# Optimization experiments

Measured on AMD Instinct MI355X. Metric: run time of the kernel, lower is better.

Reference implementation:

```python
import jax, jax.numpy as jnp
import numpy as np

DIM = 180
WS = 16        # window_size
OWS = 24       # overlap_win_size = int(16*0.5)+16
HEADS = 6
HD = DIM // HEADS
MLP_HID = DIM * 2
TABLE = (WS + OWS - 1) ** 2  # 1521
H = W = 256
B = 1


def layernorm(x, g, b, eps=1e-5):
    mu = x.mean(-1, keepdims=True)
    d = x - mu
    var = (d * d).mean(-1, keepdims=True)
    return g * d / jnp.sqrt(var + eps) + b


def setup_inputs() -> dict:
    key = jax.random.key(0)
    ks = jax.random.split(key, 12)
    std = 0.02
    inp = {
        'x': jax.random.normal(ks[0], (B, H * W, DIM), jnp.float32),
        'rpi': jax.random.randint(ks[1], (WS * WS, OWS * OWS), 0, TABLE, jnp.int32),
        'h': H,
        'w': W,
        'norm1_g': jnp.ones((DIM,), jnp.float32),
        'norm1_b': jnp.zeros((DIM,), jnp.float32),
        'q_w': jax.random.normal(ks[2], (DIM, DIM), jnp.float32) * std,
        'q_b': jnp.zeros((DIM,), jnp.float32),
        'kv_w': jax.random.normal(ks[3], (DIM, 2 * DIM), jnp.float32) * std,
        'kv_b': jnp.zeros((2 * DIM,), jnp.float32),
        'rpb_table': jax.random.normal(ks[4], (TABLE, HEADS), jnp.float32) * std,
        'proj_w': jax.random.normal(ks[5], (DIM, DIM), jnp.float32) * std,
        'proj_b': jnp.zeros((DIM,), jnp.float32),
        'norm2_g': jnp.ones((DIM,), jnp.float32),
        'norm2_b': jnp.zeros((DIM,), jnp.float32),
        'mlp_w1': jax.random.normal(ks[6], (DIM, MLP_HID), jnp.float32) * std,
        'mlp_b1': jnp.zeros((MLP_HID,), jnp.float32),
        'mlp_w2': jax.random.normal(ks[7], (MLP_HID, DIM), jnp.float32) * std,
        'mlp_b2': jnp.zeros((DIM,), jnp.float32),
    }
    return inp


def reference(x, rpi, h, w, norm1_g, norm1_b, q_w, q_b, kv_w, kv_b,
              rpb_table, proj_w, proj_b, norm2_g, norm2_b,
              mlp_w1, mlp_b1, mlp_w2, mlp_b2):
    b, L, c = x.shape
    ws, ows, heads = WS, OWS, HEADS
    d = c // heads
    scale = d ** -0.5
    pad = (ows - ws) // 2  # 4
    nh, nw = h // ws, w // ws
    nq, n = ws * ws, ows * ows
    b_ = b * nh * nw

    shortcut = x
    xn = layernorm(x, norm1_g, norm1_b)
    x_img = xn.reshape(b, h, w, c)

    q = x_img @ q_w + q_b                    # [b,h,w,c]
    kv = x_img @ kv_w + kv_b                 # [b,h,w,2c] (k | v)

    # window_partition for q -> [b_, nq, c]
    qw = q.reshape(b, nh, ws, nw, ws, c).transpose(0, 1, 3, 2, 4, 5)
    qw = qw.reshape(b_, nq, c)

    # nn.Unfold(kernel=ows, stride=ws, padding=pad) on kv -> overlapping windows
    kvp = jnp.pad(kv, ((0, 0), (pad, pad), (pad, pad), (0, 0)))
    rows = (jnp.arange(nh) * ws)[:, None] + jnp.arange(ows)   # [nh, ows]
    cols = (jnp.arange(nw) * ws)[:, None] + jnp.arange(ows)   # [nw, ows]
    t = kvp[:, rows]                         # [b, nh, ows, W+2p, 2c]
    t = t[:, :, :, cols]                     # [b, nh, ows, nw, ows, 2c]
    t = t.transpose(0, 1, 3, 2, 4, 5).reshape(b_, n, 2 * c)
    k_win, v_win = t[..., :c], t[..., c:]

    qh = qw.reshape(b_, nq, heads, d).transpose(0, 2, 1, 3) * scale
    kh = k_win.reshape(b_, n, heads, d).transpose(0, 2, 1, 3)
    vh = v_win.reshape(b_, n, heads, d).transpose(0, 2, 1, 3)

    attn = jnp.einsum('bhqd,bhkd->bhqk', qh, kh)              # [b_,heads,nq,n]
    bias = rpb_table[rpi.reshape(-1)].reshape(nq, n, heads).transpose(2, 0, 1)
    attn = jax.nn.softmax(attn + bias[None], axis=-1)
    out = jnp.einsum('bhqk,bhkd->bhqd', attn, vh)
    out = out.transpose(0, 2, 1, 3).reshape(b_, nq, c)

    # window_reverse -> [b, h*w, c]
    xo = out.reshape(b, nh, nw, ws, ws, c).transpose(0, 1, 3, 2, 4, 5)
    xo = xo.reshape(b, h * w, c)

    xo = xo @ proj_w + proj_b + shortcut
    xn2 = layernorm(xo, norm2_g, norm2_b)
    mlp = jax.nn.gelu(xn2 @ mlp_w1 + mlp_b1, approximate=False) @ mlp_w2 + mlp_b2
    return xo + mlp
```

## Files before the change

kernel.cpp:

```cpp
#include <hip/hip_runtime.h>
#include <hip/hip_bf16.h>
#include <stdint.h>

#define DIM 180
#define WS 16
#define OWS 24
#define HEADS 6
#define HD 30
#define MLP_HID 360
#define HH 256
#define WW 256
#define L (HH * WW)
#define NWIN 256
#define NQ 256
#define NK 576

#define KP1 192
#define KP2 384
#define NQKV 576

#define QSCALE 0.2633988734672831f
#define LOG2E 1.4426950408889634f

typedef float f4v __attribute__((ext_vector_type(4)));
typedef short s8v __attribute__((ext_vector_type(8)));
typedef short s4v __attribute__((ext_vector_type(4)));

static __device__ __forceinline__ short f2bf(float x) {
    union { __hip_bfloat16 h; short s; } u;
    u.h = __float2bfloat16(x);
    return u.s;
}
static __device__ __forceinline__ uint32_t pack_bf2(float lo, float hi) {
    union { __hip_bfloat162 h; uint32_t u; } u;
    u.h.x = __float2bfloat16(lo);
    u.h.y = __float2bfloat16(hi);
    return u.u;
}

typedef __attribute__((address_space(1))) const unsigned int ga_u32;
typedef __attribute__((address_space(3))) unsigned int la_u32;
static __device__ __forceinline__ void gld16(const void* g, void* l) {
    __builtin_amdgcn_global_load_lds((ga_u32*)g, (la_u32*)l, 16, 0, 0);
}

__global__ __launch_bounds__(64) void ln_kernel(const float* __restrict__ x,
                                                const float* __restrict__ g,
                                                const float* __restrict__ b,
                                                __hip_bfloat16* __restrict__ out) {
    int row = blockIdx.x;
    int t = threadIdx.x;
    const float* xr = x + (size_t)row * DIM;
    float v0 = xr[t];
    float v1 = xr[t + 64];
    float v2 = (t < DIM - 128) ? xr[t + 128] : 0.f;
    float s = v0 + v1 + v2;
    #pragma unroll
    for (int o = 32; o > 0; o >>= 1) s += __shfl_down(s, o);
    s = __shfl(s, 0);
    float mu = s * (1.f / DIM);
    float d0 = v0 - mu, d1 = v1 - mu;
    float d2 = (t < DIM - 128) ? (v2 - mu) : 0.f;
    float vs = d0 * d0 + d1 * d1 + d2 * d2;
    #pragma unroll
    for (int o = 32; o > 0; o >>= 1) vs += __shfl_down(vs, o);
    vs = __shfl(vs, 0);
    float rstd = rsqrtf(vs * (1.f / DIM) + 1e-5f);
    __hip_bfloat16* orow = out + (size_t)row * KP1;
    orow[t]      = __float2bfloat16(g[t] * d0 * rstd + b[t]);
    orow[t + 64] = __float2bfloat16(g[t + 64] * d1 * rstd + b[t + 64]);
    if (t < DIM - 128)
        orow[t + 128] = __float2bfloat16(g[t + 128] * d2 * rstd + b[t + 128]);
    if (t < KP1 - DIM) orow[DIM + t] = __float2bfloat16(0.f);
}

__global__ __launch_bounds__(256) void bias_kernel(const int* __restrict__ rpi,
                                                   const float* __restrict__ rpb,
                                                   float* __restrict__ biasC) {
    int idx = blockIdx.x * 256 + threadIdx.x;
    int j = idx & 15;
    int q = (idx >> 4) & 255;
    int r = idx >> 12;
    int kc = r % 36;
    int head = r / 36;
    int k = (kc >> 1) * 32 + ((j >> 2) << 3) + ((kc & 1) << 2) + (j & 3);
    int t = rpi[q * NK + k];
    biasC[idx] = rpb[t * HEADS + head] * LOG2E;
}

__global__ __launch_bounds__(256) void wconv_kernel(
        const float* __restrict__ qw, const float* __restrict__ kvw,
        const float* __restrict__ pw, const float* __restrict__ w1,
        const float* __restrict__ w2, short* __restrict__ wt) {
    int idx = blockIdx.x * 256 + threadIdx.x;
    float v = 0.f;
    if (idx < 110592) {
        int n = idx / KP1, k = idx - n * KP1;
        if (k < DIM) {
            if (n < DIM) v = qw[k * DIM + n] * QSCALE;
            else if (n < 540) v = kvw[k * (2 * DIM) + (n - DIM)];
        }
    } else if (idx < 147456) {
        int r = idx - 110592;
        int n = r / KP1, k = r - n * KP1;
        if (k < DIM && n < DIM) v = pw[k * DIM + n];
    } else if (idx < 221184) {
        int r = idx - 147456;
        int n = r / KP1, k = r - n * KP1;
        if (k < DIM && n < MLP_HID) v = w1[k * MLP_HID + n];
    } else {
        int r = idx - 221184;
        int n = r / KP2, k = r - n * KP2;
        if (k < MLP_HID && n < DIM) v = w2[k * DIM + n];
    }
    wt[idx] = f2bf(v);
}

__global__ __launch_bounds__(256) void bconv_kernel(
        const float* __restrict__ qb, const float* __restrict__ kvb,
        const float* __restrict__ pb, const float* __restrict__ b1,
        const float* __restrict__ b2, float* __restrict__ bv) {
    int idx = blockIdx.x * 256 + threadIdx.x;
    if (idx >= 1344) return;
    float v = 0.f;
    if (idx < 576) {
        if (idx < DIM) v = qb[idx] * QSCALE;
        else if (idx < 540) v = kvb[idx - DIM];
    } else if (idx < 768) {
        int n = idx - 576; if (n < DIM) v = pb[n];
    } else if (idx < 1152) {
        int n = idx - 768; if (n < MLP_HID) v = b1[n];
    } else {
        int n = idx - 1152; if (n < DIM) v = b2[n];
    }
    bv[idx] = v;
}

__global__ __launch_bounds__(256) void mgemm(
        const short* __restrict__ A, const short* __restrict__ Wt,
        const float* __restrict__ bias,
        float* __restrict__ outf, short* __restrict__ outb,
        int lda, int ldo, int nK, int mode) {
    __shared__ short As[2][128 * 32];
    __shared__ short Wsm[2][64 * 32];
    int tid = threadIdx.x;
    int lane = tid & 63, wave = tid >> 6;
    int q15 = lane & 15, quad = lane >> 4;
    int n0 = blockIdx.x * 64;
    int m0 = blockIdx.y * 128;

    auto stage = [&](int buf, int k0) {
        int lr = lane >> 2, c = lane & 3;
        const short* Ab = A + (size_t)m0 * lda + k0;
        #pragma unroll
        for (int i = 0; i < 2; i++) {
            int r = i * 64 + wave * 16 + lr;
            gld16(Ab + (size_t)r * lda + ((c ^ (r & 3)) * 8),
                  &As[buf][(i * 64 + wave * 16) * 32]);
        }
        const short* Wb = Wt + (size_t)n0 * lda + k0;
        {
            int r = wave * 16 + lr;
            gld16(Wb + (size_t)r * lda + ((c ^ (r & 3)) * 8),
                  &Wsm[buf][(wave * 16) * 32]);
        }
    };

    f4v acc[2][4];
    #pragma unroll
    for (int a = 0; a < 2; a++)
        #pragma unroll
        for (int b = 0; b < 4; b++) acc[a][b] = (f4v){0.f, 0.f, 0.f, 0.f};

    stage(0, 0);
    __syncthreads();
    for (int ch = 0; ch < nK; ch++) {
        int buf = ch & 1;
        if (ch + 1 < nK) stage(buf ^ 1, (ch + 1) * 32);
        s8v af[2], wf[4];
        #pragma unroll
        for (int mt = 0; mt < 2; mt++) {
            int r = wave * 32 + mt * 16 + q15;
            af[mt] = *(const s8v*)&As[buf][r * 32 + ((quad ^ (r & 3)) * 8)];
        }
        #pragma unroll
        for (int nt = 0; nt < 4; nt++) {
            int r = nt * 16 + q15;
            wf[nt] = *(const s8v*)&Wsm[buf][r * 32 + ((quad ^ (r & 3)) * 8)];
        }
        #pragma unroll
        for (int mt = 0; mt < 2; mt++)
            #pragma unroll
            for (int nt = 0; nt < 4; nt++)
                acc[mt][nt] = __builtin_amdgcn_mfma_f32_16x16x32_bf16(
                    af[mt], wf[nt], acc[mt][nt], 0, 0, 0);
        __syncthreads();
    }

    #pragma unroll
    for (int mt = 0; mt < 2; mt++) {
        int mb = m0 + wave * 32 + mt * 16 + quad * 4;
        #pragma unroll
        for (int nt = 0; nt < 4; nt++) {
            int n = n0 + nt * 16 + q15;
            float bv = bias[n];
            f4v a = acc[mt][nt];
            #pragma unroll
            for (int r = 0; r < 4; r++) {
                int m = mb + r;
                float v = a[r] + bv;
                if (mode == 0) {
                    outb[(size_t)m * ldo + n] = f2bf(v);
                } else if (mode == 1) {
                    float ge = 0.5f * v * (1.f + erff(v * 0.70710678118654752f));
                    outb[(size_t)m * ldo + n] = f2bf(ge);
                } else {
                    if (n < DIM) outf[(size_t)m * DIM + n] += v;
                }
            }
        }
    }
}

__global__ __launch_bounds__(256) void projln(
        const short* __restrict__ A, const short* __restrict__ Wt,
        const float* __restrict__ bias, const float* __restrict__ resid,
        const float* __restrict__ g2, const float* __restrict__ b2,
        float* __restrict__ outf, short* __restrict__ outb) {
    __shared__ short As[2][64 * 32];
    __shared__ short Wsm[2][192 * 32];
    int tid = threadIdx.x;
    int lane = tid & 63, wave = tid >> 6;
    int q15 = lane & 15, quad = lane >> 4;
    int m0 = blockIdx.x * 64;

    auto stage = [&](int buf, int k0) {
        int lr = lane >> 2, c = lane & 3;
        const short* Ab = A + (size_t)m0 * KP1 + k0;
        {
            int r = wave * 16 + lr;
            gld16(Ab + (size_t)r * KP1 + ((c ^ (r & 3)) * 8),
                  &As[buf][(wave * 16) * 32]);
        }
        #pragma unroll
        for (int i = 0; i < 3; i++) {
            int r = i * 64 + wave * 16 + lr;
            gld16(Wt + (size_t)r * KP1 + k0 + ((c ^ (r & 3)) * 8),
                  &Wsm[buf][(i * 64 + wave * 16) * 32]);
        }
    };

    f4v acc[12];
    #pragma unroll
    for (int b = 0; b < 12; b++) acc[b] = (f4v){0.f, 0.f, 0.f, 0.f};

    stage(0, 0);
    __syncthreads();
    for (int ch = 0; ch < KP1 / 32; ch++) {
        int buf = ch & 1;
        if (ch + 1 < KP1 / 32) stage(buf ^ 1, (ch + 1) * 32);
        int ra = wave * 16 + q15;
        s8v af = *(const s8v*)&As[buf][ra * 32 + ((quad ^ (ra & 3)) * 8)];
        #pragma unroll
        for (int nt = 0; nt < 12; nt++) {
            int r = nt * 16 + q15;
            s8v wf = *(const s8v*)&Wsm[buf][r * 32 + ((quad ^ (r & 3)) * 8)];
            acc[nt] = __builtin_amdgcn_mfma_f32_16x16x32_bf16(af, wf, acc[nt], 0, 0, 0);
        }
        __syncthreads();
    }

    float gv[12], bv[12], biasv[12];
    #pragma unroll
    for (int nt = 0; nt < 12; nt++) {
        int n = nt * 16 + q15;
        biasv[nt] = bias[n];
        gv[nt] = (n < DIM) ? g2[n] : 0.f;
        bv[nt] = (n < DIM) ? b2[n] : 0.f;
    }
    int mb = m0 + wave * 16 + quad * 4;
    #pragma unroll
    for (int r = 0; r < 4; r++) {
        int m = mb + r;
        float v[12];
        float s = 0.f, ss = 0.f;
        #pragma unroll
        for (int nt = 0; nt < 12; nt++) {
            int n = nt * 16 + q15;
            float x = acc[nt][r] + biasv[nt];
            if (n < DIM) x += resid[(size_t)m * DIM + n];
            else x = 0.f;
            v[nt] = x;
            s += x;
            ss += x * x;
        }
        #pragma unroll
        for (int o = 8; o > 0; o >>= 1) {
            s += __shfl_xor(s, o);
            ss += __shfl_xor(ss, o);
        }
        float mu = s * (1.f / DIM);
        float var = ss * (1.f / DIM) - mu * mu;
        float rstd = rsqrtf(var + 1e-5f);
        #pragma unroll
        for (int nt = 0; nt < 12; nt++) {
            int n = nt * 16 + q15;
            if (n < DIM) outf[(size_t)m * DIM + n] = v[nt];
            outb[(size_t)m * KP1 + n] = f2bf(gv[nt] * (v[nt] - mu) * rstd + bv[nt]);
        }
    }
}

#define CHUNK 32
#define NCHUNK (NK / CHUNK)

__global__ __launch_bounds__(256) void attn_kernel(
        const __hip_bfloat16* __restrict__ qkvb,
        const float* __restrict__ biasC, __hip_bfloat16* __restrict__ aout) {
    __shared__ __align__(16) short Ks[2][CHUNK][32];
    __shared__ __align__(16) short Vt[2][32][40];

    int tid = threadIdx.x;
    int lane = tid & 63;
    int wave = tid >> 6;
    int q15 = lane & 15;
    int quad = lane >> 4;
    int bid = blockIdx.x;
    int grp = bid / 48;
    int r48 = bid - grp * 48;
    int head = r48 >> 3;
    int win = grp * 8 + (r48 & 7);
    int bh = win >> 4, bw = win & 15;

    const uint32_t* kvd = (const uint32_t*)qkvb;

    s8v qf[4];
    #pragma unroll
    for (int qt = 0; qt < 4; qt++) {
        int q = wave * 64 + qt * 16 + q15;
        int qy = q >> 4, qx = q & 15;
        size_t pos = (size_t)(bh * WS + qy) * WW + (bw * WS + qx);
        const uint32_t* qp = kvd + pos * 288 + head * 15 + quad * 4;
        uint32_t w0 = qp[0], w1 = qp[1], w2 = qp[2], w3 = qp[3];
        union { uint32_t u[4]; s8v v; } cv;
        cv.u[0] = w0; cv.u[1] = w1; cv.u[2] = w2; cv.u[3] = w3;
        qf[qt] = cv.v;
    }
    if (head == 0) {
        int qy = tid >> 4, qx = tid & 15;
        size_t pos = (size_t)(bh * WS + qy) * WW + (bw * WS + qx);
        uint2 z = make_uint2(0u, 0u);
        uint2* oz = (uint2*)(aout + pos * KP1 + DIM);
        oz[0] = z; oz[1] = z; oz[2] = z;
    }

    int keyK = tid >> 3, pK = tid & 7;
    int keyV = tid & 31, pp = tid >> 5;

    auto rowbase = [&](int jk) -> const uint32_t* {
        int oy = jk / OWS, ox = jk - oy * OWS;
        int y = bh * WS - 4 + oy, x = bw * WS - 4 + ox;
        if ((unsigned)y < HH && (unsigned)x < WW)
            return kvd + ((size_t)y * WW + x) * 288;
        return nullptr;
    };
    auto loadKV = [&](int c0, uint32_t& ka, uint32_t& kb, uint32_t& va, uint32_t& vb) {
        ka = kb = va = vb = 0u;
        const uint32_t* rk = rowbase(c0 + keyK);
        if (rk) {
            const uint32_t* kp = rk + 90 + head * 15 + pK * 2;
            ka = kp[0];
            if (pK < 7) kb = kp[1];
        }
        const uint32_t* rv = rowbase(c0 + keyV);
        if (rv) {
            const uint32_t* vp = rv + 180 + head * 15 + pp * 2;
            va = vp[0];
            if (pp < 7) vb = vp[1];
        }
    };
    auto writeKV = [&](int bufi, uint32_t ka, uint32_t kb, uint32_t va, uint32_t vb) {
        *(uint2*)&Ks[bufi][keyK][pK * 4] = make_uint2(ka, kb);
        int d0 = pp * 4;
        Vt[bufi][d0][keyV]     = (short)(va & 0xffff);
        Vt[bufi][d0 + 1][keyV] = (short)(va >> 16);
        if (pp < 7) {
            Vt[bufi][d0 + 2][keyV] = (short)(vb & 0xffff);
            Vt[bufi][d0 + 3][keyV] = (short)(vb >> 16);
        } else {
            Vt[bufi][30][keyV] = (short)0x3F80;
            Vt[bufi][31][keyV] = 0;
        }
    };

    const float* bC  = biasC + (size_t)head * (36 * 256 * 16);
    const float* bCl = bC + ((size_t)(wave * 64 + q15)) * 16 + quad * 4;
    f4v cb[2][4];
    auto loadBias = [&](int ch) {
        #pragma unroll
        for (int kt = 0; kt < 2; kt++)
            #pragma unroll
            for (int qt = 0; qt < 4; qt++)
                cb[kt][qt] = *(const f4v*)(bCl + ((size_t)(ch * 2 + kt) * 256 + qt * 16) * 16);
    };

    uint32_t kaA, kbA, vaA, vbA;
    uint32_t kaB, kbB, vaB, vbB;

    loadKV(0,     kaA, kbA, vaA, vbA);
    loadKV(CHUNK, kaB, kbB, vaB, vbB);
    loadBias(0);
    writeKV(0, kaA, kbA, vaA, vbA);
    __syncthreads();

    f4v oacc[2][4];
    #pragma unroll
    for (int a = 0; a < 2; a++)
        #pragma unroll
        for (int b = 0; b < 4; b++) oacc[a][b] = (f4v){0.f, 0.f, 0.f, 0.f};

    int pr = ((q15 & 12) << 1) | (q15 & 3);

    auto body = [&](int ch, int bufR,
                    uint32_t& kaR, uint32_t& kbR, uint32_t& vaR, uint32_t& vbR,
                    uint32_t& kaW, uint32_t& kbW, uint32_t& vaW, uint32_t& vbW) {
        s8v kf0 = *(const s8v*)&Ks[bufR][pr][quad * 8];
        s8v kf1 = *(const s8v*)&Ks[bufR][pr + 4][quad * 8];
        s8v va0 = *(const s8v*)&Vt[bufR][q15][quad * 8];
        s8v va1 = *(const s8v*)&Vt[bufR][16 + q15][quad * 8];

        #pragma unroll
        for (int qt = 0; qt < 4; qt++) {
            cb[0][qt] = __builtin_amdgcn_mfma_f32_16x16x32_bf16(kf0, qf[qt], cb[0][qt], 0, 0, 0);
            cb[1][qt] = __builtin_amdgcn_mfma_f32_16x16x32_bf16(kf1, qf[qt], cb[1][qt], 0, 0, 0);
        }
        if (ch + 2 < NCHUNK) loadKV((ch + 2) * CHUNK, kaR, kbR, vaR, vbR);

        s8v pbv[4];
        #pragma unroll
        for (int qt = 0; qt < 4; qt++) {
            union { uint32_t u[4]; s8v v; } pk;
            pk.u[0] = pack_bf2(__builtin_amdgcn_exp2f(cb[0][qt][0]), __builtin_amdgcn_exp2f(cb[0][qt][1]));
            pk.u[1] = pack_bf2(__builtin_amdgcn_exp2f(cb[0][qt][2]), __builtin_amdgcn_exp2f(cb[0][qt][3]));
            pk.u[2] = pack_bf2(__builtin_amdgcn_exp2f(cb[1][qt][0]), __builtin_amdgcn_exp2f(cb[1][qt][1]));
            pk.u[3] = pack_bf2(__builtin_amdgcn_exp2f(cb[1][qt][2]), __builtin_amdgcn_exp2f(cb[1][qt][3]));
            pbv[qt] = pk.v;
        }
        if (ch + 1 < NCHUNK) loadBias(ch + 1);

        #pragma unroll
        for (int qt = 0; qt < 4; qt++) {
            oacc[0][qt] = __builtin_amdgcn_mfma_f32_16x16x32_bf16(va0, pbv[qt], oacc[0][qt], 0, 0, 0);
            oacc[1][qt] = __builtin_amdgcn_mfma_f32_16x16x32_bf16(va1, pbv[qt], oacc[1][qt], 0, 0, 0);
        }

        if (ch + 1 < NCHUNK) writeKV(bufR ^ 1, kaW, kbW, vaW, vbW);

        asm volatile("s_waitcnt lgkmcnt(0)" ::: "memory");
        __builtin_amdgcn_sched_barrier(0);
        __builtin_amdgcn_s_barrier();
    };

    #pragma unroll 1
    for (int t = 0; t < NCHUNK / 2; t++) {
        body(2 * t,     0, kaA, kbA, vaA, vbA, kaB, kbB, vaB, vbB);
        body(2 * t + 1, 1, kaB, kbB, vaB, vbB, kaA, kbA, vaA, vbA);
    }

    #pragma unroll
    for (int nt = 0; nt < 4; nt++) {
        float l = __shfl(oacc[1][nt][2], 48 | q15);
        float rl = 1.0f / l;
        int q = wave * 64 + nt * 16 + q15;
        int qy = q >> 4, qx = q & 15;
        size_t pos = (size_t)(bh * WS + qy) * WW + (bw * WS + qx);
        uint32_t* od = (uint32_t*)(aout + pos * KP1 + head * HD);
        int dh = quad * 2;
        f4v o0 = oacc[0][nt], o1 = oacc[1][nt];
        od[dh]     = pack_bf2(o0[0] * rl, o0[1] * rl);
        od[dh + 1] = pack_bf2(o0[2] * rl, o0[3] * rl);
        od[8 + dh] = pack_bf2(o1[0] * rl, o1[1] * rl);
        if (quad < 3)
            od[8 + dh + 1] = pack_bf2(o1[2] * rl, o1[3] * rl);
    }
}

extern "C" void kernel_launch(void* const* d_in, const int* in_sizes, int n_in,
                              void* d_out, int out_size, void* d_ws, size_t ws_size,
                              hipStream_t stream) {
    const float* x      = (const float*)d_in[0];
    const int*   rpi    = (const int*)d_in[1];
    const float* n1g    = (const float*)d_in[4];
    const float* n1b    = (const float*)d_in[5];
    const float* q_w    = (const float*)d_in[6];
    const float* q_b    = (const float*)d_in[7];
    const float* kv_w   = (const float*)d_in[8];
    const float* kv_b   = (const float*)d_in[9];
    const float* rpb    = (const float*)d_in[10];
    const float* proj_w = (const float*)d_in[11];
    const float* proj_b = (const float*)d_in[12];
    const float* n2g    = (const float*)d_in[13];
    const float* n2b    = (const float*)d_in[14];
    const float* w1     = (const float*)d_in[15];
    const float* b1     = (const float*)d_in[16];
    const float* w2     = (const float*)d_in[17];
    const float* b2     = (const float*)d_in[18];
    float* out = (float*)d_out;

    char* ws = (char*)d_ws;
    short* qkvb  = (short*)(ws);
    short* xn    = (short*)(ws + 75497472ull);
    float* biasC = (float*)(ws + 100663296ull);
    short* wt    = (short*)(ws + 104202240ull);
    short* wt_qkv  = wt;
    short* wt_proj = wt + 110592;
    short* wt_1    = wt + 147456;
    short* wt_2    = wt + 221184;
    float* bvec  = (float*)(ws + 104202240ull + 589824ull);
    float* b_qkv  = bvec;
    float* b_proj = bvec + 576;
    float* b_1    = bvec + 768;
    float* b_2    = bvec + 1152;
    short* ao  = xn;
    short* xn2 = qkvb;
    short* h1  = qkvb + 12582912;

    bias_kernel<<<884736 / 256, 256, 0, stream>>>(rpi, rpb, biasC);
    wconv_kernel<<<294912 / 256, 256, 0, stream>>>(q_w, kv_w, proj_w, w1, w2, wt);
    bconv_kernel<<<6, 256, 0, stream>>>(q_b, kv_b, proj_b, b1, b2, bvec);
    ln_kernel<<<L, 64, 0, stream>>>(x, n1g, n1b, (__hip_bfloat16*)xn);
    mgemm<<<dim3(NQKV / 64, L / 128), 256, 0, stream>>>(
        xn, wt_qkv, b_qkv, nullptr, qkvb, KP1, NQKV, KP1 / 32, 0);
    attn_kernel<<<NWIN * HEADS, 256, 0, stream>>>(
        (const __hip_bfloat16*)qkvb, biasC, (__hip_bfloat16*)ao);
    projln<<<L / 64, 256, 0, stream>>>(
        ao, wt_proj, b_proj, x, n2g, n2b, out, xn2);
    mgemm<<<dim3(KP2 / 64, L / 128), 256, 0, stream>>>(
        xn2, wt_1, b_1, nullptr, h1, KP1, KP2, KP1 / 32, 1);
    mgemm<<<dim3(KP1 / 64, L / 128), 256, 0, stream>>>(
        h1, wt_2, b_2, out, nullptr, KP2, 0, KP2 / 32, 3);
}
```

Before: 411.7 us.

## Widen attention to 512 threads, bf16 bias, tanh GELU, batched layernorm

The attention kernel now runs 8 waves of 32 queries each and processes 64-key chunks. The K shared-memory layout gets an XOR swizzle and the bias is added after the QK MFMA instead of being used as the accumulator. The precomputed bias table is stored as bf16, halving its traffic. GELU switches from exact erf to the tanh approximation computed with exp2, and layernorm packs four rows per 256-thread block. The tanh GELU and bf16 bias add numerical error relative to the exact reference.

```diff
diff --git a/kernel.cpp b/kernel.cpp
--- a/kernel.cpp
+++ b/kernel.cpp
@@ -37,6 +37,12 @@
     u.h.y = __float2bfloat16(hi);
     return u.u;
 }
+static __device__ __forceinline__ float bflo(uint32_t u) {
+    union { uint32_t i; float f; } c; c.i = u << 16; return c.f;
+}
+static __device__ __forceinline__ float bfhi(uint32_t u) {
+    union { uint32_t i; float f; } c; c.i = u & 0xffff0000u; return c.f;
+}
 
 typedef __attribute__((address_space(1))) const unsigned int ga_u32;
 typedef __attribute__((address_space(3))) unsigned int la_u32;
@@ -44,12 +50,12 @@
     __builtin_amdgcn_global_load_lds((ga_u32*)g, (la_u32*)l, 16, 0, 0);
 }
 
-__global__ __launch_bounds__(64) void ln_kernel(const float* __restrict__ x,
-                                                const float* __restrict__ g,
-                                                const float* __restrict__ b,
-                                                __hip_bfloat16* __restrict__ out) {
-    int row = blockIdx.x;
-    int t = threadIdx.x;
+__global__ __launch_bounds__(256) void ln_kernel(const float* __restrict__ x,
+                                                 const float* __restrict__ g,
+                                                 const float* __restrict__ b,
+                                                 __hip_bfloat16* __restrict__ out) {
+    int row = blockIdx.x * 4 + (threadIdx.x >> 6);
+    int t = threadIdx.x & 63;
     const float* xr = x + (size_t)row * DIM;
     float v0 = xr[t];
     float v1 = xr[t + 64];
@@ -76,7 +82,7 @@
 
 __global__ __launch_bounds__(256) void bias_kernel(const int* __restrict__ rpi,
                                                    const float* __restrict__ rpb,
-                                                   float* __restrict__ biasC) {
+                                                   ushort* __restrict__ biasC) {
     int idx = blockIdx.x * 256 + threadIdx.x;
     int j = idx & 15;
     int q = (idx >> 4) & 255;
@@ -85,7 +91,7 @@
     int head = r / 36;
     int k = (kc >> 1) * 32 + ((j >> 2) << 3) + ((kc & 1) << 2) + (j & 3);
     int t = rpi[q * NK + k];
-    biasC[idx] = rpb[t * HEADS + head] * LOG2E;
+    biasC[idx] = (ushort)f2bf(rpb[t * HEADS + head] * LOG2E);
 }
 
 __global__ __launch_bounds__(256) void wconv_kernel(
@@ -212,8 +218,10 @@
                 if (mode == 0) {
                     outb[(size_t)m * ldo + n] = f2bf(v);
                 } else if (mode == 1) {
-                    float ge = 0.5f * v * (1.f + erff(v * 0.70710678118654752f));
-                    outb[(size_t)m * ldo + n] = f2bf(ge);
+                    float y = 0.7978845608028654f * (v + 0.044715f * v * v * v);
+                    float e = __builtin_amdgcn_exp2f(y * 2.885390081777927f);
+                    float th = 1.f - 2.f / (1.f + e);
+                    outb[(size_t)m * ldo + n] = f2bf(0.5f * v * (1.f + th));
                 } else {
                     if (n < DIM) outf[(size_t)m * DIM + n] += v;
                 }
@@ -311,14 +319,14 @@
     }
 }
 
-#define CHUNK 32
+#define CHUNK 64
 #define NCHUNK (NK / CHUNK)
 
-__global__ __launch_bounds__(256) void attn_kernel(
+__global__ __launch_bounds__(512) void attn_kernel(
         const __hip_bfloat16* __restrict__ qkvb,
-        const float* __restrict__ biasC, __hip_bfloat16* __restrict__ aout) {
+        const ushort* __restrict__ biasC, __hip_bfloat16* __restrict__ aout) {
     __shared__ __align__(16) short Ks[2][CHUNK][32];
-    __shared__ __align__(16) short Vt[2][32][40];
+    __shared__ __align__(16) short Vt[2][2][32][40];
 
     int tid = threadIdx.x;
     int lane = tid & 63;
@@ -334,10 +342,10 @@
 
     const uint32_t* kvd = (const uint32_t*)qkvb;
 
-    s8v qf[4];
-    #pragma unroll
-    for (int qt = 0; qt < 4; qt++) {
-        int q = wave * 64 + qt * 16 + q15;
+    s8v qf[2];
+    #pragma unroll
+    for (int qt = 0; qt < 2; qt++) {
+        int q = wave * 32 + qt * 16 + q15;
         int qy = q >> 4, qx = q & 15;
         size_t pos = (size_t)(bh * WS + qy) * WW + (bw * WS + qx);
         const uint32_t* qp = kvd + pos * 288 + head * 15 + quad * 4;
@@ -346,7 +354,7 @@
         cv.u[0] = w0; cv.u[1] = w1; cv.u[2] = w2; cv.u[3] = w3;
         qf[qt] = cv.v;
     }
-    if (head == 0) {
+    if (head == 0 && tid < 256) {
         int qy = tid >> 4, qx = tid & 15;
         size_t pos = (size_t)(bh * WS + qy) * WW + (bw * WS + qx);
         uint2 z = make_uint2(0u, 0u);
@@ -355,7 +363,9 @@
     }
 
     int keyK = tid >> 3, pK = tid & 7;
-    int keyV = tid & 31, pp = tid >> 5;
+    int keyV = tid & 63, pp = tid >> 6;
+    int gV = keyV >> 5, kv32 = keyV & 31;
+    int pKs = pK ^ (((keyK >> 3) & 3) << 1);
 
     auto rowbase = [&](int jk) -> const uint32_t* {
         int oy = jk / OWS, ox = jk - oy * OWS;
@@ -380,28 +390,28 @@
         }
     };
     auto writeKV = [&](int bufi, uint32_t ka, uint32_t kb, uint32_t va, uint32_t vb) {
-        *(uint2*)&Ks[bufi][keyK][pK * 4] = make_uint2(ka, kb);
+        *(uint2*)&Ks[bufi][keyK][pKs * 4] = make_uint2(ka, kb);
         int d0 = pp * 4;
-        Vt[bufi][d0][keyV]     = (short)(va & 0xffff);
-        Vt[bufi][d0 + 1][keyV] = (short)(va >> 16);
+        Vt[bufi][gV][d0][kv32]     = (short)(va & 0xffff);
+        Vt[bufi][gV][d0 + 1][kv32] = (short)(va >> 16);
         if (pp < 7) {
-            Vt[bufi][d0 + 2][keyV] = (short)(vb & 0xffff);
-            Vt[bufi][d0 + 3][keyV] = (short)(vb >> 16);
+            Vt[bufi][gV][d0 + 2][kv32] = (short)(vb & 0xffff);
+            Vt[bufi][gV][d0 + 3][kv32] = (short)(vb >> 16);
         } else {
-            Vt[bufi][30][keyV] = (short)0x3F80;
-            Vt[bufi][31][keyV] = 0;
-        }
-    };
-
-    const float* bC  = biasC + (size_t)head * (36 * 256 * 16);
-    const float* bCl = bC + ((size_t)(wave * 64 + q15)) * 16 + quad * 4;
-    f4v cb[2][4];
+            Vt[bufi][gV][30][kv32] = (short)0x3F80;
+            Vt[bufi][gV][31][kv32] = 0;
+        }
+    };
+
+    const char* bBase = (const char*)biasC +
+        ((size_t)head * (36 * 256 * 16) + (size_t)(wave * 32 + q15) * 16 + quad * 4) * 2;
+    uint2 bb[4][2];
     auto loadBias = [&](int ch) {
         #pragma unroll
-        for (int kt = 0; kt < 2; kt++)
+        for (int kt = 0; kt < 4; kt++)
             #pragma unroll
-            for (int qt = 0; qt < 4; qt++)
-                cb[kt][qt] = *(const f4v*)(bCl + ((size_t)(ch * 2 + kt) * 256 + qt * 16) * 16);
+            for (int qt = 0; qt < 2; qt++)
+                bb[kt][qt] = *(const uint2*)(bBase + (size_t)(ch * 4 + kt) * 8192 + qt * 512);
     };
 
     uint32_t kaA, kbA, vaA, vbA;
@@ -413,46 +423,66 @@
     writeKV(0, kaA, kbA, vaA, vbA);
     __syncthreads();
 
-    f4v oacc[2][4];
+    f4v oacc[2][2];
     #pragma unroll
     for (int a = 0; a < 2; a++)
         #pragma unroll
-        for (int b = 0; b < 4; b++) oacc[a][b] = (f4v){0.f, 0.f, 0.f, 0.f};
+        for (int b = 0; b < 2; b++) oacc[a][b] = (f4v){0.f, 0.f, 0.f, 0.f};
 
     int pr = ((q15 & 12) << 1) | (q15 & 3);
+    int rslot = (quad ^ (q15 >> 2)) * 8;
 
     auto body = [&](int ch, int bufR,
                     uint32_t& kaR, uint32_t& kbR, uint32_t& vaR, uint32_t& vbR,
                     uint32_t& kaW, uint32_t& kbW, uint32_t& vaW, uint32_t& vbW) {
-        s8v kf0 = *(const s8v*)&Ks[bufR][pr][quad * 8];
-        s8v kf1 = *(const s8v*)&Ks[bufR][pr + 4][quad * 8];
-        s8v va0 = *(const s8v*)&Vt[bufR][q15][quad * 8];
-        s8v va1 = *(const s8v*)&Vt[bufR][16 + q15][quad * 8];
-
-        #pragma unroll
-        for (int qt = 0; qt < 4; qt++) {
-            cb[0][qt] = __builtin_amdgcn_mfma_f32_16x16x32_bf16(kf0, qf[qt], cb[0][qt], 0, 0, 0);
-            cb[1][qt] = __builtin_amdgcn_mfma_f32_16x16x32_bf16(kf1, qf[qt], cb[1][qt], 0, 0, 0);
-        }
+        s8v kf[4];
+        #pragma unroll
+        for (int kt = 0; kt < 4; kt++)
+            kf[kt] = *(const s8v*)&Ks[bufR][(kt >> 1) * 32 + pr + (kt & 1) * 4][rslot];
+        s8v va[2][2];
+        #pragma unroll
+        for (int g = 0; g < 2; g++) {
+            va[0][g] = *(const s8v*)&Vt[bufR][g][q15][quad * 8];
+            va[1][g] = *(const s8v*)&Vt[bufR][g][16 + q15][quad * 8];
+        }
+
+        f4v zf = (f4v){0.f, 0.f, 0.f, 0.f};
+        f4v s[2][4];
+        #pragma unroll
+        for (int qt = 0; qt < 2; qt++)
+            #pragma unroll
+            for (int kt = 0; kt < 4; kt++)
+                s[qt][kt] = __builtin_amdgcn_mfma_f32_16x16x32_bf16(kf[kt], qf[qt], zf, 0, 0, 0);
+
         if (ch + 2 < NCHUNK) loadKV((ch + 2) * CHUNK, kaR, kbR, vaR, vbR);
 
-        s8v pbv[4];
-        #pragma unroll
-        for (int qt = 0; qt < 4; qt++) {
-            union { uint32_t u[4]; s8v v; } pk;
-            pk.u[0] = pack_bf2(__builtin_amdgcn_exp2f(cb[0][qt][0]), __builtin_amdgcn_exp2f(cb[0][qt][1]));
-            pk.u[1] = pack_bf2(__builtin_amdgcn_exp2f(cb[0][qt][2]), __builtin_amdgcn_exp2f(cb[0][qt][3]));
-            pk.u[2] = pack_bf2(__builtin_amdgcn_exp2f(cb[1][qt][0]), __builtin_amdgcn_exp2f(cb[1][qt][1]));
-            pk.u[3] = pack_bf2(__builtin_amdgcn_exp2f(cb[1][qt][2]), __builtin_amdgcn_exp2f(cb[1][qt][3]));
-            pbv[qt] = pk.v;
-        }
+        s8v pbv[2][2];
+        #pragma unroll
+        for (int qt = 0; qt < 2; qt++)
+            #pragma unroll
+            for (int g = 0; g < 2; g++) {
+                f4v c0 = s[qt][g * 2], c1 = s[qt][g * 2 + 1];
+                uint2 b0 = bb[g * 2][qt], b1 = bb[g * 2 + 1][qt];
+                union { uint32_t u[4]; s8v v; } pk;
+                pk.u[0] = pack_bf2(__builtin_amdgcn_exp2f(c0[0] + bflo(b0.x)),
+                                   __builtin_amdgcn_exp2f(c0[1] + bfhi(b0.x)));
+                pk.u[1] = pack_bf2(__builtin_amdgcn_exp2f(c0[2] + bflo(b0.y)),
+                                   __builtin_amdgcn_exp2f(c0[3] + bfhi(b0.y)));
+                pk.u[2] = pack_bf2(__builtin_amdgcn_exp2f(c1[0] + bflo(b1.x)),
+                                   __builtin_amdgcn_exp2f(c1[1] + bfhi(b1.x)));
+                pk.u[3] = pack_bf2(__builtin_amdgcn_exp2f(c1[2] + bflo(b1.y)),
+                                   __builtin_amdgcn_exp2f(c1[3] + bfhi(b1.y)));
+                pbv[qt][g] = pk.v;
+            }
         if (ch + 1 < NCHUNK) loadBias(ch + 1);
 
         #pragma unroll
-        for (int qt = 0; qt < 4; qt++) {
-            oacc[0][qt] = __builtin_amdgcn_mfma_f32_16x16x32_bf16(va0, pbv[qt], oacc[0][qt], 0, 0, 0);
-            oacc[1][qt] = __builtin_amdgcn_mfma_f32_16x16x32_bf16(va1, pbv[qt], oacc[1][qt], 0, 0, 0);
-        }
+        for (int qt = 0; qt < 2; qt++)
+            #pragma unroll
+            for (int dt = 0; dt < 2; dt++) {
+                oacc[dt][qt] = __builtin_amdgcn_mfma_f32_16x16x32_bf16(va[dt][0], pbv[qt][0], oacc[dt][qt], 0, 0, 0);
+                oacc[dt][qt] = __builtin_amdgcn_mfma_f32_16x16x32_bf16(va[dt][1], pbv[qt][1], oacc[dt][qt], 0, 0, 0);
+            }
 
         if (ch + 1 < NCHUNK) writeKV(bufR ^ 1, kaW, kbW, vaW, vbW);
 
@@ -462,21 +492,22 @@
     };
 
     #pragma unroll 1
-    for (int t = 0; t < NCHUNK / 2; t++) {
+    for (int t = 0; t < 4; t++) {
         body(2 * t,     0, kaA, kbA, vaA, vbA, kaB, kbB, vaB, vbB);
         body(2 * t + 1, 1, kaB, kbB, vaB, vbB, kaA, kbA, vaA, vbA);
     }
-
-    #pragma unroll
-    for (int nt = 0; nt < 4; nt++) {
-        float l = __shfl(oacc[1][nt][2], 48 | q15);
+    body(8, 0, kaA, kbA, vaA, vbA, kaB, kbB, vaB, vbB);
+
+    #pragma unroll
+    for (int qt = 0; qt < 2; qt++) {
+        float l = __shfl(oacc[1][qt][2], 48 | q15);
         float rl = 1.0f / l;
-        int q = wave * 64 + nt * 16 + q15;
+        int q = wave * 32 + qt * 16 + q15;
         int qy = q >> 4, qx = q & 15;
         size_t pos = (size_t)(bh * WS + qy) * WW + (bw * WS + qx);
         uint32_t* od = (uint32_t*)(aout + pos * KP1 + head * HD);
         int dh = quad * 2;
-        f4v o0 = oacc[0][nt], o1 = oacc[1][nt];
+        f4v o0 = oacc[0][qt], o1 = oacc[1][qt];
         od[dh]     = pack_bf2(o0[0] * rl, o0[1] * rl);
         od[dh + 1] = pack_bf2(o0[2] * rl, o0[3] * rl);
         od[8 + dh] = pack_bf2(o1[0] * rl, o1[1] * rl);
@@ -510,7 +541,7 @@
     char* ws = (char*)d_ws;
     short* qkvb  = (short*)(ws);
     short* xn    = (short*)(ws + 75497472ull);
-    float* biasC = (float*)(ws + 100663296ull);
+    ushort* biasC = (ushort*)(ws + 100663296ull);
     short* wt    = (short*)(ws + 104202240ull);
     short* wt_qkv  = wt;
     short* wt_proj = wt + 110592;
@@ -528,10 +559,10 @@
     bias_kernel<<<884736 / 256, 256, 0, stream>>>(rpi, rpb, biasC);
     wconv_kernel<<<294912 / 256, 256, 0, stream>>>(q_w, kv_w, proj_w, w1, w2, wt);
     bconv_kernel<<<6, 256, 0, stream>>>(q_b, kv_b, proj_b, b1, b2, bvec);
-    ln_kernel<<<L, 64, 0, stream>>>(x, n1g, n1b, (__hip_bfloat16*)xn);
+    ln_kernel<<<L / 4, 256, 0, stream>>>(x, n1g, n1b, (__hip_bfloat16*)xn);
     mgemm<<<dim3(NQKV / 64, L / 128), 256, 0, stream>>>(
         xn, wt_qkv, b_qkv, nullptr, qkvb, KP1, NQKV, KP1 / 32, 0);
-    attn_kernel<<<NWIN * HEADS, 256, 0, stream>>>(
+    attn_kernel<<<NWIN * HEADS, 512, 0, stream>>>(
         (const __hip_bfloat16*)qkvb, biasC, (__hip_bfloat16*)ao);
     projln<<<L / 64, 256, 0, stream>>>(
         ao, wt_proj, b_proj, x, n2g, n2b, out, xn2);
```

Measured after the change: 412.7 us. No clear change (+0.2%).
